# Performance work log

Measured on AMD Instinct MI355X. Metric: run time of the kernel, lower is better.

## Reference

```python
import jax, jax.numpy as jnp
import numpy as np

NX, NTEST, DX, DY = 8192, 8192, 32, 32
VAR_EPS = 0.01   # params['var_eps']
L_MEAN = 8.0     # fit kernel lengthscale after l_scale adjustment
L_VAR = 8.0


def _rbf(X, Y, l):
    # pairwise squared distances: [Nx, Nq]
    d2 = (jnp.sum(X * X, axis=1)[:, None]
          + jnp.sum(Y * Y, axis=1)[None, :]
          - 2.0 * (X @ Y.T))
    return jnp.exp(-jnp.maximum(d2, 0.0) / (2.0 * l * l))


def setup_inputs() -> dict:
    key = jax.random.key(0)
    ks = jax.random.split(key, 10)
    inp = {
        'x_mu':   jax.random.normal(ks[0], (NTEST, DX), jnp.float32),
        'y_eta':  jax.random.normal(ks[1], (NTEST, DY), jnp.float32),
        'y_mean': jax.random.normal(ks[2], (NTEST, DY), jnp.float32),
        'y_var':  jax.random.normal(ks[3], (NTEST, DY), jnp.float32) * 0.1,
        'X_mean': jax.random.normal(ks[4], (NX, DX + DY), jnp.float32),
        'X_var':  jax.random.normal(ks[5], (NX, DX + 2 * DY), jnp.float32),
        'Z_mean': jax.random.normal(ks[6], (NX, DY), jnp.float32),
        'Z_var':  jax.random.normal(ks[7], (NX, DY), jnp.float32),
        # precomputed inverse Gram matrices (stand-ins with same compute pattern)
        'kXXmean_inv': jax.random.normal(ks[8], (NX, NX), jnp.float32) * 0.001,
        'kXXvar_inv':  jax.random.normal(ks[9], (NX, NX), jnp.float32) * 0.001,
    }
    return inp


def reference(x_mu, y_eta, y_mean, y_var, X_mean, X_var, Z_mean, Z_var,
              kXXmean_inv, kXXvar_inv):
    # map_mean: x_mean = [x_mu, y_mean + y_var]
    x_mean = jnp.concatenate([x_mu, y_mean + y_var], axis=1)          # [Nq, DX+DY]
    Lambda_mean = kXXmean_inv @ Z_mean                                # [Nx, DY]
    z_mean = _rbf(X_mean, x_mean, L_MEAN).T @ Lambda_mean             # [Nq, DY]

    # map_var: x_var = [x_mu, var_eps * flip(y_eta), y_mean + y_var]
    x_var = jnp.concatenate(
        [x_mu, VAR_EPS * jnp.flip(y_eta, axis=0), y_mean + y_var], axis=1)
    Lambda_var = kXXvar_inv @ Z_var                                   # [Nx, DY]
    z_var = _rbf(X_var, x_var, L_VAR).T @ Lambda_var                  # [Nq, DY]

    # transported sample: (y_mean + z_mean) + (y_var + z_var)
    return (y_mean + z_mean) + (y_var + z_var)
```

## Files before the change

### kernel.cpp

```cpp
#include <hip/hip_runtime.h>
#include <stdint.h>

#define NXR 8192
#define NQR 8192
#define DMEAN 64
#define DVAR 96
#define DYC 32

typedef float f32x4 __attribute__((ext_vector_type(4)));
typedef __bf16 bf16x8 __attribute__((ext_vector_type(8)));
typedef unsigned short us4v __attribute__((ext_vector_type(4)));

__device__ __forceinline__ unsigned short f2bf(float f) {
    union { float f; uint32_t u; } v; v.f = f;
    uint32_t r = (v.u + 0x7FFFu + ((v.u >> 16) & 1u)) >> 16;
    return (unsigned short)r;
}
__device__ __forceinline__ float bf2f(unsigned short b) {
    union { uint32_t u; float f; } v; v.u = ((uint32_t)b) << 16;
    return v.f;
}
__device__ __forceinline__ int perm_idx(int k, int c) {
    return (k >> 5) * 1024 + (c >> 4) * 512 +
           ((((k >> 3) & 3) * 16 + (c & 15)) * 8) + (k & 7);
}

__global__ __launch_bounds__(256) void k_prep(
    const float* __restrict__ x_mu, const float* __restrict__ y_eta,
    const float* __restrict__ y_mean, const float* __restrict__ y_var,
    const float* __restrict__ X_mean, const float* __restrict__ X_var,
    const float* __restrict__ Z_mean, const float* __restrict__ Z_var,
    unsigned short* __restrict__ Qm, unsigned short* __restrict__ Qv,
    unsigned short* __restrict__ Xm, unsigned short* __restrict__ Xv,
    unsigned short* __restrict__ Zpm, unsigned short* __restrict__ Zpv,
    float* __restrict__ qn_m, float* __restrict__ qn_v,
    float* __restrict__ Xn_m, float* __restrict__ Xn_v,
    float* __restrict__ lam_f32, float* __restrict__ out)
{
    int tid = blockIdx.x * 256 + threadIdx.x;
    lam_f32[tid] = 0.0f;
    int w = threadIdx.x >> 6;
    int lane = threadIdx.x & 63;
    int row = blockIdx.x * 4 + w;

    float accq_m = 0.f, accq_v = 0.f;
    if (lane < 32) {
        int c = lane;
        float xm = x_mu[row * 32 + c];
        float s  = y_mean[row * 32 + c] + y_var[row * 32 + c];
        float e  = 0.01f * y_eta[(NQR - 1 - row) * 32 + c];
        unsigned short bx = f2bf(xm), bs = f2bf(s), be = f2bf(e);
        Qm[row * DMEAN + c] = bx;  Qm[row * DMEAN + 32 + c] = bs;
        Qv[row * DVAR + c] = bx;   Qv[row * DVAR + 32 + c] = be;
        Qv[row * DVAR + 64 + c] = bs;
        out[row * 32 + c] = s;
        Zpm[perm_idx(row, c)] = f2bf(Z_mean[row * 32 + c]);
        Zpv[perm_idx(row, c)] = f2bf(Z_var[row * 32 + c]);
        float fx = bf2f(bx), fs = bf2f(bs), fe = bf2f(be);
        accq_m = fx * fx + fs * fs;
        accq_v = fx * fx + fe * fe + fs * fs;
    }
    float a = X_mean[row * DMEAN + lane];
    unsigned short ba = f2bf(a);
    Xm[row * DMEAN + lane] = ba;
    float fa = bf2f(ba);
    float accx_m = fa * fa;

    float b0 = X_var[row * DVAR + lane];
    unsigned short bb0 = f2bf(b0);
    Xv[row * DVAR + lane] = bb0;
    float fb0 = bf2f(bb0);
    float accx_v = fb0 * fb0;
    if (lane < 32) {
        float b1 = X_var[row * DVAR + 64 + lane];
        unsigned short bb1 = f2bf(b1);
        Xv[row * DVAR + 64 + lane] = bb1;
        float fb1 = bf2f(bb1);
        accx_v += fb1 * fb1;
    }
    for (int o = 32; o >= 1; o >>= 1) {
        accq_m += __shfl_xor(accq_m, o, 64);
        accq_v += __shfl_xor(accq_v, o, 64);
        accx_m += __shfl_xor(accx_m, o, 64);
        accx_v += __shfl_xor(accx_v, o, 64);
    }
    if (lane == 0) {
        qn_m[row] = accq_m; qn_v[row] = accq_v;
        Xn_m[row] = accx_m; Xn_v[row] = accx_v;
    }
}

__global__ __launch_bounds__(256) void k_lambda(
    const float* __restrict__ kXXm, const float* __restrict__ kXXv,
    const unsigned short* __restrict__ Zpm, const unsigned short* __restrict__ Zpv,
    float* __restrict__ lam_f32)
{
    int b = blockIdx.x;
    int mat = b & 1;
    int split = (b >> 1) & 1;
    int rb = b >> 2;
    const float* A = mat ? kXXv : kXXm;
    const unsigned short* Zp = mat ? Zpv : Zpm;
    float* lam = lam_f32 + mat * (NXR * DYC);

    int w = threadIdx.x >> 6, lane = threadIdx.x & 63;
    int r0 = rb * 64 + w * 16;
    int arow = r0 + (lane & 15);
    int kgrp = (lane >> 4) * 8;
    const float* Arow = A + (size_t)arow * NXR;

    f32x4 acc0 = {0.f, 0.f, 0.f, 0.f}, acc1 = {0.f, 0.f, 0.f, 0.f};
#pragma unroll 2
    for (int kb = 0; kb < 128; ++kb) {
        int kbase = split * 4096 + kb * 32;
        int k = kbase + kgrp;
        const f32x4* p = (const f32x4*)(Arow + k);
        f32x4 a0 = p[0], a1 = p[1];
        union { unsigned short u[8]; bf16x8 v; } af;
#pragma unroll
        for (int j = 0; j < 4; ++j) { af.u[j] = f2bf(a0[j]); af.u[4 + j] = f2bf(a1[j]); }
        const unsigned short* zb = Zp + (size_t)(kbase >> 5) * 1024 + lane * 8;
        bf16x8 bz0 = *(const bf16x8*)(zb);
        bf16x8 bz1 = *(const bf16x8*)(zb + 512);
        acc0 = __builtin_amdgcn_mfma_f32_16x16x32_bf16(af.v, bz0, acc0, 0, 0, 0);
        acc1 = __builtin_amdgcn_mfma_f32_16x16x32_bf16(af.v, bz1, acc1, 0, 0, 0);
    }
    int rbase = r0 + (lane >> 4) * 4;
    int c0 = lane & 15;
#pragma unroll
    for (int r = 0; r < 4; ++r) {
        atomicAdd(&lam[(rbase + r) * DYC + c0], acc0[r]);
        atomicAdd(&lam[(rbase + r) * DYC + c0 + 16], acc1[r]);
    }
}

__global__ __launch_bounds__(256) void k_pack(
    const float* __restrict__ lam_f32,
    unsigned short* __restrict__ Lpm, unsigned short* __restrict__ Lpv)
{
    int t = blockIdx.x * 256 + threadIdx.x;
    int mat = t >> 18;
    int rem = t & 262143;
    int x = rem >> 5, c = rem & 31;
    unsigned short v = f2bf(lam_f32[t]);
    (mat ? Lpv : Lpm)[perm_idx(x, c)] = v;
}

__global__ __launch_bounds__(256) void k_transport(
    const unsigned short* __restrict__ Qm, const unsigned short* __restrict__ Qv,
    const unsigned short* __restrict__ Xm, const unsigned short* __restrict__ Xv,
    const float* __restrict__ qn_m, const float* __restrict__ qn_v,
    const float* __restrict__ Xn_m, const float* __restrict__ Xn_v,
    const unsigned short* __restrict__ Lpm, const unsigned short* __restrict__ Lpv,
    float* __restrict__ out)
{
    __shared__ unsigned short KT[4][16 * 40];
    int b = blockIdx.x;
    int mat = b & 1;
    int split = (b >> 1) & 3;
    int qb = b >> 3;
    const unsigned short* Q = mat ? Qv : Qm;
    const unsigned short* X = mat ? Xv : Xm;
    const float* qn = mat ? qn_v : qn_m;
    const float* Xn = mat ? Xn_v : Xn_m;
    const unsigned short* Lp = mat ? Lpv : Lpm;
    const int D = mat ? DVAR : DMEAN;
    const int nk0 = mat ? 3 : 2;

    int w = threadIdx.x >> 6, lane = threadIdx.x & 63;
    int q0 = qb * 64 + w * 16;
    int qrow = q0 + (lane & 15);
    int g = lane >> 4;

    bf16x8 Qf[3];
    for (int c0 = 0; c0 < nk0; ++c0)
        Qf[c0] = *(const bf16x8*)(Q + (size_t)qrow * D + c0 * 32 + g * 8);
    float qn_c = qn[qrow];
    unsigned short* lds = KT[w];

    f32x4 z0 = {0.f, 0.f, 0.f, 0.f}, z1 = {0.f, 0.f, 0.f, 0.f};
    for (int xb = 0; xb < 64; ++xb) {
        int x0 = split * 2048 + xb * 32;
#pragma unroll
        for (int sub = 0; sub < 2; ++sub) {
            int xrow = x0 + sub * 16 + (lane & 15);
            const unsigned short* Xr = X + (size_t)xrow * D + g * 8;
            f32x4 s = {0.f, 0.f, 0.f, 0.f};
            s = __builtin_amdgcn_mfma_f32_16x16x32_bf16(*(const bf16x8*)(Xr), Qf[0], s, 0, 0, 0);
            s = __builtin_amdgcn_mfma_f32_16x16x32_bf16(*(const bf16x8*)(Xr + 32), Qf[1], s, 0, 0, 0);
            if (nk0 == 3)
                s = __builtin_amdgcn_mfma_f32_16x16x32_bf16(*(const bf16x8*)(Xr + 64), Qf[2], s, 0, 0, 0);
            int xnb = x0 + sub * 16 + g * 4;
            f32x4 xn4 = *(const f32x4*)(Xn + xnb);
            us4v kv;
#pragma unroll
            for (int r = 0; r < 4; ++r) {
                float d2 = xn4[r] + qn_c - 2.0f * s[r];
                d2 = fmaxf(d2, 0.0f);
                kv[r] = f2bf(__expf(-d2 * 0.0078125f));
            }
            *(us4v*)(lds + (lane & 15) * 40 + sub * 16 + g * 4) = kv;
        }
        asm volatile("s_waitcnt lgkmcnt(0)" ::: "memory");
        bf16x8 Kf = *(const bf16x8*)(lds + (lane & 15) * 40 + g * 8);
        const unsigned short* lpb = Lp + (size_t)(x0 >> 5) * 1024 + lane * 8;
        bf16x8 l0 = *(const bf16x8*)(lpb);
        bf16x8 l1 = *(const bf16x8*)(lpb + 512);
        z0 = __builtin_amdgcn_mfma_f32_16x16x32_bf16(Kf, l0, z0, 0, 0, 0);
        z1 = __builtin_amdgcn_mfma_f32_16x16x32_bf16(Kf, l1, z1, 0, 0, 0);
    }
    int rbase = q0 + g * 4;
    int c0 = lane & 15;
#pragma unroll
    for (int r = 0; r < 4; ++r) {
        atomicAdd(&out[(rbase + r) * 32 + c0], z0[r]);
        atomicAdd(&out[(rbase + r) * 32 + c0 + 16], z1[r]);
    }
}

extern "C" void kernel_launch(void* const* d_in, const int* in_sizes, int n_in,
                              void* d_out, int out_size, void* d_ws, size_t ws_size,
                              hipStream_t stream) {
    const float* x_mu   = (const float*)d_in[0];
    const float* y_eta  = (const float*)d_in[1];
    const float* y_mean = (const float*)d_in[2];
    const float* y_var  = (const float*)d_in[3];
    const float* X_mean = (const float*)d_in[4];
    const float* X_var  = (const float*)d_in[5];
    const float* Z_mean = (const float*)d_in[6];
    const float* Z_var  = (const float*)d_in[7];
    const float* kXXm   = (const float*)d_in[8];
    const float* kXXv   = (const float*)d_in[9];
    float* out = (float*)d_out;

    char* ws = (char*)d_ws;
    size_t off = 0;
    auto carve = [&](size_t bytes) { char* p = ws + off; off += (bytes + 255) & ~(size_t)255; return p; };
    unsigned short* Qm  = (unsigned short*)carve(NQR * DMEAN * 2);
    unsigned short* Qv  = (unsigned short*)carve(NQR * DVAR * 2);
    unsigned short* Xm  = (unsigned short*)carve(NXR * DMEAN * 2);
    unsigned short* Xv  = (unsigned short*)carve(NXR * DVAR * 2);
    unsigned short* Zpm = (unsigned short*)carve(NXR * DYC * 2);
    unsigned short* Zpv = (unsigned short*)carve(NXR * DYC * 2);
    unsigned short* Lpm = (unsigned short*)carve(NXR * DYC * 2);
    unsigned short* Lpv = (unsigned short*)carve(NXR * DYC * 2);
    float* qn_m = (float*)carve(NQR * 4);
    float* qn_v = (float*)carve(NQR * 4);
    float* Xn_m = (float*)carve(NXR * 4);
    float* Xn_v = (float*)carve(NXR * 4);
    float* lam_f32 = (float*)carve(2 * NXR * DYC * 4);

    k_prep<<<dim3(2048), dim3(256), 0, stream>>>(
        x_mu, y_eta, y_mean, y_var, X_mean, X_var, Z_mean, Z_var,
        Qm, Qv, Xm, Xv, Zpm, Zpv, qn_m, qn_v, Xn_m, Xn_v, lam_f32, out);
    k_lambda<<<dim3(512), dim3(256), 0, stream>>>(kXXm, kXXv, Zpm, Zpv, lam_f32);
    k_pack<<<dim3(2048), dim3(256), 0, stream>>>(lam_f32, Lpm, Lpv);
    k_transport<<<dim3(1024), dim3(256), 0, stream>>>(
        Qm, Qv, Xm, Xv, qn_m, qn_v, Xn_m, Xn_v, Lpm, Lpv, out);
}
```

Baseline: 716.3 us.

## Restructure lambda GEMM with in-block K-split reduction, double-buffered loads, fused pack

The lambda matvec kernel now gives each block 16 rows, with its four waves splitting K and reducing through shared memory. This replaces the global fp32 atomics, the zeroing pass in prep and the separate pack kernel, and the result is written straight into the permuted bf16 layout. The A-matrix loads are double-buffered in registers so global loads overlap the conversion and MFMA work, and the launch bounds request higher occupancy. The cost is more registers for the buffers and a block-wide sync before the reduction.

```diff
diff --git a/kernel.cpp b/kernel.cpp
--- a/kernel.cpp
+++ b/kernel.cpp
@@ -35,10 +35,8 @@
     unsigned short* __restrict__ Zpm, unsigned short* __restrict__ Zpv,
     float* __restrict__ qn_m, float* __restrict__ qn_v,
     float* __restrict__ Xn_m, float* __restrict__ Xn_v,
-    float* __restrict__ lam_f32, float* __restrict__ out)
+    float* __restrict__ out)
 {
-    int tid = blockIdx.x * 256 + threadIdx.x;
-    lam_f32[tid] = 0.0f;
     int w = threadIdx.x >> 6;
     int lane = threadIdx.x & 63;
     int row = blockIdx.x * 4 + w;
@@ -90,60 +88,78 @@
     }
 }
 
-__global__ __launch_bounds__(256) void k_lambda(
+__global__ __launch_bounds__(256, 4) void k_lambda(
     const float* __restrict__ kXXm, const float* __restrict__ kXXv,
     const unsigned short* __restrict__ Zpm, const unsigned short* __restrict__ Zpv,
-    float* __restrict__ lam_f32)
+    unsigned short* __restrict__ Lpm, unsigned short* __restrict__ Lpv)
 {
+    __shared__ float red[4][64][8];
     int b = blockIdx.x;
     int mat = b & 1;
-    int split = (b >> 1) & 1;
-    int rb = b >> 2;
+    int rg = b >> 1;
     const float* A = mat ? kXXv : kXXm;
     const unsigned short* Zp = mat ? Zpv : Zpm;
-    float* lam = lam_f32 + mat * (NXR * DYC);
+    unsigned short* Lp = mat ? Lpv : Lpm;
 
     int w = threadIdx.x >> 6, lane = threadIdx.x & 63;
-    int r0 = rb * 64 + w * 16;
+    int r0 = rg * 16;
     int arow = r0 + (lane & 15);
     int kgrp = (lane >> 4) * 8;
     const float* Arow = A + (size_t)arow * NXR;
 
     f32x4 acc0 = {0.f, 0.f, 0.f, 0.f}, acc1 = {0.f, 0.f, 0.f, 0.f};
-#pragma unroll 2
-    for (int kb = 0; kb < 128; ++kb) {
-        int kbase = split * 4096 + kb * 32;
-        int k = kbase + kgrp;
-        const f32x4* p = (const f32x4*)(Arow + k);
-        f32x4 a0 = p[0], a1 = p[1];
-        union { unsigned short u[8]; bf16x8 v; } af;
-#pragma unroll
-        for (int j = 0; j < 4; ++j) { af.u[j] = f2bf(a0[j]); af.u[4 + j] = f2bf(a1[j]); }
-        const unsigned short* zb = Zp + (size_t)(kbase >> 5) * 1024 + lane * 8;
-        bf16x8 bz0 = *(const bf16x8*)(zb);
-        bf16x8 bz1 = *(const bf16x8*)(zb + 512);
-        acc0 = __builtin_amdgcn_mfma_f32_16x16x32_bf16(af.v, bz0, acc0, 0, 0, 0);
-        acc1 = __builtin_amdgcn_mfma_f32_16x16x32_bf16(af.v, bz1, acc1, 0, 0, 0);
-    }
-    int rbase = r0 + (lane >> 4) * 4;
-    int c0 = lane & 15;
-#pragma unroll
-    for (int r = 0; r < 4; ++r) {
-        atomicAdd(&lam[(rbase + r) * DYC + c0], acc0[r]);
-        atomicAdd(&lam[(rbase + r) * DYC + c0 + 16], acc1[r]);
-    }
-}
-
-__global__ __launch_bounds__(256) void k_pack(
-    const float* __restrict__ lam_f32,
-    unsigned short* __restrict__ Lpm, unsigned short* __restrict__ Lpv)
-{
-    int t = blockIdx.x * 256 + threadIdx.x;
-    int mat = t >> 18;
-    int rem = t & 262143;
-    int x = rem >> 5, c = rem & 31;
-    unsigned short v = f2bf(lam_f32[t]);
-    (mat ? Lpv : Lpm)[perm_idx(x, c)] = v;
+    f32x4 bA[4][2], bB[4][2];
+    int kb = w * 64;
+
+#define LOAD_BODY(BUF, KB0) do { \
+    _Pragma("unroll") \
+    for (int j = 0; j < 4; ++j) { \
+        const f32x4* p = (const f32x4*)(Arow + (((KB0) + j) << 5) + kgrp); \
+        BUF[j][0] = p[0]; BUF[j][1] = p[1]; \
+    } } while (0)
+
+#define PROC_BODY(BUF, KB0) do { \
+    _Pragma("unroll") \
+    for (int j = 0; j < 4; ++j) { \
+        union { unsigned short u[8]; bf16x8 v; } af; \
+        _Pragma("unroll") \
+        for (int q2 = 0; q2 < 4; ++q2) { \
+            af.u[q2] = f2bf(BUF[j][0][q2]); af.u[4 + q2] = f2bf(BUF[j][1][q2]); \
+        } \
+        const unsigned short* zb = Zp + (((size_t)((KB0) + j)) << 10) + lane * 8; \
+        bf16x8 bz0 = *(const bf16x8*)(zb); \
+        bf16x8 bz1 = *(const bf16x8*)(zb + 512); \
+        acc0 = __builtin_amdgcn_mfma_f32_16x16x32_bf16(af.v, bz0, acc0, 0, 0, 0); \
+        acc1 = __builtin_amdgcn_mfma_f32_16x16x32_bf16(af.v, bz1, acc1, 0, 0, 0); \
+    } } while (0)
+
+    LOAD_BODY(bA, kb);
+#pragma unroll 1
+    for (int s = 0; s < 7; ++s) {
+        LOAD_BODY(bB, kb + 4);
+        PROC_BODY(bA, kb);
+        LOAD_BODY(bA, kb + 8);
+        PROC_BODY(bB, kb + 4);
+        kb += 8;
+    }
+    LOAD_BODY(bB, kb + 4);
+    PROC_BODY(bA, kb);
+    PROC_BODY(bB, kb + 4);
+#undef LOAD_BODY
+#undef PROC_BODY
+
+    *(f32x4*)&red[w][lane][0] = acc0;
+    *(f32x4*)&red[w][lane][4] = acc1;
+    __syncthreads();
+    int t = threadIdx.x;
+    int row = t >> 4, c16 = t & 15;
+    int ls = (row >> 2) * 16 + c16;
+    int rr = row & 3;
+    float v0 = red[0][ls][rr] + red[1][ls][rr] + red[2][ls][rr] + red[3][ls][rr];
+    float v1 = red[0][ls][4 + rr] + red[1][ls][4 + rr] +
+               red[2][ls][4 + rr] + red[3][ls][4 + rr];
+    Lp[perm_idx(r0 + row, c16)]      = f2bf(v0);
+    Lp[perm_idx(r0 + row, c16 + 16)] = f2bf(v1);
 }
 
 __global__ __launch_bounds__(256) void k_transport(
@@ -248,13 +264,11 @@
     float* qn_v = (float*)carve(NQR * 4);
     float* Xn_m = (float*)carve(NXR * 4);
     float* Xn_v = (float*)carve(NXR * 4);
-    float* lam_f32 = (float*)carve(2 * NXR * DYC * 4);
 
     k_prep<<<dim3(2048), dim3(256), 0, stream>>>(
         x_mu, y_eta, y_mean, y_var, X_mean, X_var, Z_mean, Z_var,
-        Qm, Qv, Xm, Xv, Zpm, Zpv, qn_m, qn_v, Xn_m, Xn_v, lam_f32, out);
-    k_lambda<<<dim3(512), dim3(256), 0, stream>>>(kXXm, kXXv, Zpm, Zpv, lam_f32);
-    k_pack<<<dim3(2048), dim3(256), 0, stream>>>(lam_f32, Lpm, Lpv);
+        Qm, Qv, Xm, Xv, Zpm, Zpv, qn_m, qn_v, Xn_m, Xn_v, out);
+    k_lambda<<<dim3(1024), dim3(256), 0, stream>>>(kXXm, kXXv, Zpm, Zpv, Lpm, Lpv);
     k_transport<<<dim3(1024), dim3(256), 0, stream>>>(
         Qm, Qv, Xm, Xv, qn_m, qn_v, Xn_m, Xn_v, Lpm, Lpv, out);
 }
```

Measured after the change: 716.0 us. No clear change (-0.0%).
